# Optimization experiments

Measured on AMD Instinct MI355X. Metric: run time of the kernel, lower is better.

Reference implementation:

```python
import jax, jax.numpy as jnp
import numpy as np

N, C, D, G, FC0, FC1, TOPK = 1024, 2, 1024, 16, 64, 16, 10
DG = D // G  # 64, per-group dim for WQ/WK
OPG = D // G  # 64, conv output channels per group (dim[2]=1024, groups=16)


def setup_inputs() -> dict:
    key = jax.random.key(0)
    ks = jax.random.split(key, 11)
    s = 0.02
    return {
        "f_a": jax.random.normal(ks[0], (N, C, D), jnp.float32),
        "position_embedding": jax.random.uniform(ks[1], (C, N, N, FC0), jnp.float32),
        "iou": jax.random.uniform(ks[2], (C, N, N), jnp.float32),
        "WG_w": jax.random.normal(ks[3], (FC1, FC0), jnp.float32) * s,
        "WG_b": jnp.zeros((FC1,), jnp.float32),
        "WK_w": jax.random.normal(ks[4], (D, D), jnp.float32) * s,
        "WK_b": jnp.zeros((D,), jnp.float32),
        "WQ_w": jax.random.normal(ks[5], (D, D), jnp.float32) * s,
        "WQ_b": jnp.zeros((D,), jnp.float32),
        "conv_w": jax.random.normal(ks[6], (D, D), jnp.float32) * s,  # [out=1024, in_per_group=1024] (1x1 kernel squeezed)
        "conv_b": jnp.zeros((D,), jnp.float32),
    }


def reference(f_a, position_embedding, iou, WG_w, WG_b, WK_w, WK_b, WQ_w, WQ_b, conv_w, conv_b):
    n = f_a.shape[0]
    k = min(n, TOPK)
    fa = jnp.transpose(f_a, (1, 0, 2))  # [C, N, D]

    # geometric bias: relu(Linear) -> [C, N, N, G] -> [C, G, N, N]
    w_g = jax.nn.relu(jnp.einsum('cmne,oe->cmno', position_embedding, WG_w) + WG_b)
    w_g = jnp.transpose(w_g, (0, 3, 1, 2))  # [C, G, N, N]

    # multi-head Q/K with per-group dim DG
    w_k = (jnp.einsum('cnd,ed->cne', fa, WK_w) + WK_b).reshape(C, n, G, DG)
    w_q = (jnp.einsum('cnd,ed->cne', fa, WQ_w) + WQ_b).reshape(C, n, G, DG)
    aff = jnp.einsum('cngd,cmgd->cgnm', w_q, w_k) / jnp.sqrt(jnp.float32(DG))  # [C, G, N, N]

    # iou_method == 'b': iou >= 1e-6 -> log(1)=0, else log(1e-6)
    log_iou = jnp.where(iou >= 1e-6, jnp.float32(0.0), jnp.log(jnp.float32(1e-6)))[:, None, :, :]

    w_mn = jnp.log(jnp.clip(w_g, 1e-6, None)) + aff + log_iou  # [C, G, N, N]

    # topk -> softmax over topk -> scatter back into dense [C, G, N, N]
    vals, idx = jax.lax.top_k(w_mn, k)
    soft = jax.nn.softmax(vals, axis=-1)
    ci = jnp.arange(C)[:, None, None, None]
    gi = jnp.arange(G)[None, :, None, None]
    ri = jnp.arange(n)[None, None, :, None]
    attn = jnp.zeros_like(w_mn).at[ci, gi, ri, idx].set(soft)

    # sparse attention-weighted aggregation of values
    out = jnp.einsum('cgnm,cmd->cgnd', attn, fa)  # [C, G, N, D]

    # grouped 1x1 conv: group g maps its D input channels to OPG output channels
    Wr = conv_w.reshape(G, OPG, D)  # [g, o_local, i]
    y = jnp.einsum('goi,cgni->ncgo', Wr, out).reshape(n, C, G * OPG) + conv_b  # [N, C, 1024]
    return y
```

## Files before the change

kernel.cpp:

```cpp
#include <hip/hip_runtime.h>
#include <math.h>

#define NT 1024
#define CD 2
#define DD 1024
#define GG 16
#define LOG1E6 -13.8155105579642740f
#define NEG_BIG -1e30f

typedef short bf16x8 __attribute__((ext_vector_type(8)));
typedef float f32x4  __attribute__((ext_vector_type(4)));

__device__ __forceinline__ unsigned short bf16_rne(float x) {
    unsigned int u = __float_as_uint(x);
    unsigned int r = (u + 0x7fffu + ((u >> 16) & 1u)) >> 16;
    return (unsigned short)r;
}

__device__ __forceinline__ void split3_8(const float* v, bf16x8& h, bf16x8& m, bf16x8& l) {
    #pragma unroll
    for (int e = 0; e < 8; ++e) {
        const float x = v[e];
        const unsigned short hb = bf16_rne(x);
        const float hf = __uint_as_float((unsigned int)hb << 16);
        const float r1 = x - hf;
        const unsigned short mb = bf16_rne(r1);
        const float mf = __uint_as_float((unsigned int)mb << 16);
        const float r2 = r1 - mf;
        const unsigned short lb = bf16_rne(r2);
        h[e] = (short)hb; m[e] = (short)mb; l[e] = (short)lb;
    }
}

__global__ __launch_bounds__(256) void k1_proj(
    const float* __restrict__ fa,
    const float* __restrict__ Wq, const float* __restrict__ bq,
    const float* __restrict__ Wk, const float* __restrict__ bk,
    const float* __restrict__ Wc, const float* __restrict__ bc,
    float* __restrict__ Qo, float* __restrict__ Ko, float* __restrict__ Vo)
{
    const int et = blockIdx.x, rt = blockIdx.y, z = blockIdx.z;
    const float* W  = (z == 0) ? Wq : (z == 1) ? Wk : Wc;
    const float* bb = (z == 0) ? bq : (z == 1) ? bk : bc;
    float* Out      = (z == 0) ? Qo : (z == 1) ? Ko : Vo;

    __shared__ float Al[32][132];
    __shared__ float Wl[32][68];

    const int t  = threadIdx.x;
    const int tx = t & 15, ty = t >> 4;
    const int dd = t & 7,  rr = t >> 3;
    const int r0 = rt * 128, e0 = et * 64;

    float acc[8][4];
    #pragma unroll
    for (int a = 0; a < 8; ++a)
        #pragma unroll
        for (int b = 0; b < 4; ++b) acc[a][b] = 0.f;

    for (int kt = 0; kt < 32; ++kt) {
        const int db = kt * 32 + dd * 4;
        #pragma unroll
        for (int p = 0; p < 4; ++p) {
            const int row = rr + p * 32;
            const int r = r0 + row;
            const int n = r & (NT - 1), c = r >> 10;
            float4 a4 = *(const float4*)&fa[((size_t)(n * CD + c)) * DD + db];
            Al[dd*4+0][row] = a4.x; Al[dd*4+1][row] = a4.y;
            Al[dd*4+2][row] = a4.z; Al[dd*4+3][row] = a4.w;
        }
        #pragma unroll
        for (int p = 0; p < 2; ++p) {
            const int erow = rr + p * 32;
            float4 w4 = *(const float4*)&W[((size_t)(e0 + erow)) * DD + db];
            Wl[dd*4+0][erow] = w4.x; Wl[dd*4+1][erow] = w4.y;
            Wl[dd*4+2][erow] = w4.z; Wl[dd*4+3][erow] = w4.w;
        }
        __syncthreads();
        #pragma unroll 4
        for (int d = 0; d < 32; ++d) {
            float4 a0 = *(const float4*)&Al[d][ty * 8];
            float4 a1 = *(const float4*)&Al[d][ty * 8 + 4];
            float4 w4 = *(const float4*)&Wl[d][tx * 4];
            float av[8] = {a0.x, a0.y, a0.z, a0.w, a1.x, a1.y, a1.z, a1.w};
            float wv[4] = {w4.x, w4.y, w4.z, w4.w};
            #pragma unroll
            for (int a = 0; a < 8; ++a)
                #pragma unroll
                for (int b = 0; b < 4; ++b) acc[a][b] += av[a] * wv[b];
        }
        __syncthreads();
    }
    float4 b4 = *(const float4*)&bb[e0 + tx * 4];
    #pragma unroll
    for (int a = 0; a < 8; ++a) {
        float4 o;
        o.x = acc[a][0] + b4.x; o.y = acc[a][1] + b4.y;
        o.z = acc[a][2] + b4.z; o.w = acc[a][3] + b4.w;
        *(float4*)&Out[((size_t)(r0 + ty * 8 + a)) * DD + e0 + tx * 4] = o;
    }
}

__global__ __launch_bounds__(256) void k2a_aff(
    const float* __restrict__ Q, const float* __restrict__ Km,
    float* __restrict__ aff)
{
    const int jt = blockIdx.x, it = blockIdx.y, cg = blockIdx.z;
    const int c = cg >> 4, g = cg & 15;
    __shared__ float Ql[64][68];
    __shared__ float Kl[64][68];
    const int t = threadIdx.x;
    const int dd = t & 15, rr = t >> 4;
    const int i0 = it * 64, j0 = jt * 64;
    #pragma unroll
    for (int p = 0; p < 4; ++p) {
        const int row = rr + p * 16;
        float4 q4 = *(const float4*)&Q[((size_t)(c * NT + i0 + row)) * DD + g * 64 + dd * 4];
        Ql[dd*4+0][row] = q4.x; Ql[dd*4+1][row] = q4.y;
        Ql[dd*4+2][row] = q4.z; Ql[dd*4+3][row] = q4.w;
        float4 k4 = *(const float4*)&Km[((size_t)(c * NT + j0 + row)) * DD + g * 64 + dd * 4];
        Kl[dd*4+0][row] = k4.x; Kl[dd*4+1][row] = k4.y;
        Kl[dd*4+2][row] = k4.z; Kl[dd*4+3][row] = k4.w;
    }
    __syncthreads();
    const int tx = t & 15, ty = t >> 4;
    float acc[4][4];
    #pragma unroll
    for (int a = 0; a < 4; ++a)
        #pragma unroll
        for (int b = 0; b < 4; ++b) acc[a][b] = 0.f;
    #pragma unroll 8
    for (int d = 0; d < 64; ++d) {
        float4 q4 = *(const float4*)&Ql[d][ty * 4];
        float4 k4 = *(const float4*)&Kl[d][tx * 4];
        float qv[4] = {q4.x, q4.y, q4.z, q4.w};
        float kv[4] = {k4.x, k4.y, k4.z, k4.w};
        #pragma unroll
        for (int a = 0; a < 4; ++a)
            #pragma unroll
            for (int b = 0; b < 4; ++b) acc[a][b] += qv[a] * kv[b];
    }
    #pragma unroll
    for (int a = 0; a < 4; ++a) {
        float4 o;
        o.x = acc[a][0] * 0.125f; o.y = acc[a][1] * 0.125f;
        o.z = acc[a][2] * 0.125f; o.w = acc[a][3] * 0.125f;
        *(float4*)&aff[(((size_t)(c * GG + g)) * NT + i0 + ty * 4 + a) * NT + j0 + tx * 4] = o;
    }
}

__global__ __launch_bounds__(256, 4) void k3_scan(
    const float* __restrict__ pe, const float* __restrict__ iou,
    const float* __restrict__ WGw, const float* __restrict__ WGb,
    const float* __restrict__ aff,
    float* __restrict__ cv, int* __restrict__ ci)
{
    const int ch = blockIdx.x;
    const int it = blockIdx.y;
    const int c  = blockIdx.z;
    const int i0 = it * 8;

    __shared__ float wgl[8][16][33];
    __shared__ float ios[8][33];

    const int t = threadIdx.x;
    const int wave = t >> 6, lane = t & 63;
    const int lg = lane & 15, lk = lane >> 4;
    const int p_i = t >> 5, jq = t & 31;
    const int s_i = t >> 5, s_g = (t >> 1) & 15, s_h = t & 1;

    bf16x8 bh[2], bm[2], bl[2];
    #pragma unroll
    for (int kp = 0; kp < 2; ++kp) {
        float w8[8];
        float4 w0 = *(const float4*)&WGw[lg * 64 + kp * 32 + lk * 8];
        float4 w1 = *(const float4*)&WGw[lg * 64 + kp * 32 + lk * 8 + 4];
        w8[0]=w0.x; w8[1]=w0.y; w8[2]=w0.z; w8[3]=w0.w;
        w8[4]=w1.x; w8[5]=w1.y; w8[6]=w1.z; w8[7]=w1.w;
        split3_8(w8, bh[kp], bm[kp], bl[kp]);
    }
    const float bias = WGb[lg];

    float tv[10]; int tidx[10];
    #pragma unroll
    for (int q = 0; q < 10; ++q) { tv[q] = NEG_BIG; tidx[q] = 0; }

    for (int s = 0; s < 8; ++s) {
        const int j0 = ch * 256 + s * 32;
        {
            const float ia = iou[((size_t)c * NT + (i0 + p_i)) * NT + j0 + jq];
            ios[p_i][jq] = (ia >= 1e-6f) ? 0.f : LOG1E6;
        }
        #pragma unroll 1
        for (int rtt = 0; rtt < 4; ++rtt) {
            const int rt = wave * 4 + rtt;
            const int ib = rt >> 1;
            const int jb = (rt & 1) * 16;
            const float* pr = &pe[(((size_t)c * NT + (i0 + ib)) * NT + (j0 + jb + lg)) * 64];
            f32x4 acc = {0.f, 0.f, 0.f, 0.f};
            #pragma unroll
            for (int kp = 0; kp < 2; ++kp) {
                float a8[8];
                float4 v0 = *(const float4*)&pr[kp * 32 + lk * 8];
                float4 v1 = *(const float4*)&pr[kp * 32 + lk * 8 + 4];
                a8[0]=v0.x; a8[1]=v0.y; a8[2]=v0.z; a8[3]=v0.w;
                a8[4]=v1.x; a8[5]=v1.y; a8[6]=v1.z; a8[7]=v1.w;
                bf16x8 ah, am, al;
                split3_8(a8, ah, am, al);
                acc = __builtin_amdgcn_mfma_f32_16x16x32_bf16(al, bh[kp], acc, 0, 0, 0);
                acc = __builtin_amdgcn_mfma_f32_16x16x32_bf16(ah, bl[kp], acc, 0, 0, 0);
                acc = __builtin_amdgcn_mfma_f32_16x16x32_bf16(am, bm[kp], acc, 0, 0, 0);
                acc = __builtin_amdgcn_mfma_f32_16x16x32_bf16(am, bh[kp], acc, 0, 0, 0);
                acc = __builtin_amdgcn_mfma_f32_16x16x32_bf16(ah, bm[kp], acc, 0, 0, 0);
                acc = __builtin_amdgcn_mfma_f32_16x16x32_bf16(ah, bh[kp], acc, 0, 0, 0);
            }
            #pragma unroll
            for (int q = 0; q < 4; ++q) {
                const float v = acc[q] + bias;
                wgl[ib][lg][jb + lk * 4 + q] = (v > 1e-6f) ? __logf(v) : LOG1E6;
            }
        }
        __syncthreads();
        {
            const float* ar = &aff[(((size_t)(c * GG + s_g)) * NT + (i0 + s_i)) * NT + j0 + s_h * 16];
            const float* wl = &wgl[s_i][s_g][s_h * 16];
            const float* il = &ios[s_i][s_h * 16];
            #pragma unroll
            for (int j4 = 0; j4 < 16; j4 += 4) {
                float4 a4 = *(const float4*)&ar[j4];
                float av[4] = {a4.x, a4.y, a4.z, a4.w};
                #pragma unroll
                for (int q = 0; q < 4; ++q) {
                    const float val = wl[j4 + q] + av[q] + il[j4 + q];
                    if (val > tv[0]) {
                        const int ix = j0 + s_h * 16 + j4 + q;
                        #pragma unroll
                        for (int sl = 0; sl < 10; ++sl) {
                            const bool up   = (sl < 9) ? (val > tv[sl + 1]) : false;
                            const bool here = (val > tv[sl]);
                            const float ntv = up ? tv[sl + 1] : (here ? val : tv[sl]);
                            const int   nti = up ? tidx[sl + 1] : (here ? ix : tidx[sl]);
                            tv[sl] = ntv; tidx[sl] = nti;
                        }
                    }
                }
            }
        }
        __syncthreads();
    }

    float* mv = &wgl[0][0][0];
    int*   mi = (int*)(mv + 1280);
    const int pair = t >> 1;
    if (s_h == 1) {
        #pragma unroll
        for (int q = 0; q < 10; ++q) { mv[pair * 10 + q] = tv[q]; mi[pair * 10 + q] = tidx[q]; }
    }
    __syncthreads();
    if (s_h == 0) {
        for (int q = 9; q >= 0; --q) {
            const float val = mv[pair * 10 + q];
            const int   ix  = mi[pair * 10 + q];
            if (val > tv[0]) {
                #pragma unroll
                for (int sl = 0; sl < 10; ++sl) {
                    const bool up   = (sl < 9) ? (val > tv[sl + 1]) : false;
                    const bool here = (val > tv[sl]);
                    const float ntv = up ? tv[sl + 1] : (here ? val : tv[sl]);
                    const int   nti = up ? tidx[sl + 1] : (here ? ix : tidx[sl]);
                    tv[sl] = ntv; tidx[sl] = nti;
                }
            }
        }
        const size_t base = ((((size_t)c * NT + (i0 + s_i)) * GG + s_g) * 4 + ch) * 10;
        #pragma unroll
        for (int q = 0; q < 10; ++q) { cv[base + q] = tv[q]; ci[base + q] = tidx[q]; }
    }
}

__global__ __launch_bounds__(256) void k2b2_fin(
    const float* __restrict__ cv, const int* __restrict__ ci,
    const float* __restrict__ V, float* __restrict__ y)
{
    const int w    = (blockIdx.x << 2) + (threadIdx.x >> 6);
    const int lane = threadIdx.x & 63;
    const int c = w >> 14;
    const int i = (w >> 4) & (NT - 1);
    const int g = w & 15;

    float tv[10]; int tidx[10];
    #pragma unroll
    for (int q = 0; q < 10; ++q) { tv[q] = NEG_BIG; tidx[q] = 0; }

    const size_t base = (size_t)w * 40;
    for (int chn = 0; chn < 4; ++chn) {
        const float* cvp = &cv[base + chn * 10];
        const int*   cip = &ci[base + chn * 10];
        for (int q = 9; q >= 0; --q) {
            const float val = cvp[q];
            const int   ix  = cip[q];
            if (val > tv[0]) {
                #pragma unroll
                for (int sl = 0; sl < 10; ++sl) {
                    const bool up   = (sl < 9) ? (val > tv[sl + 1]) : false;
                    const bool here = (val > tv[sl]);
                    const float ntv = up ? tv[sl + 1] : (here ? val : tv[sl]);
                    const int   nti = up ? tidx[sl + 1] : (here ? ix : tidx[sl]);
                    tv[sl] = ntv; tidx[sl] = nti;
                }
            }
        }
    }
    const float m = tv[9];
    float wgt[10]; float sm = 0.f;
    #pragma unroll
    for (int q = 0; q < 10; ++q) { wgt[q] = __expf(tv[q] - m); sm += wgt[q]; }
    const float inv = 1.f / sm;
    float o = 0.f;
    #pragma unroll
    for (int q = 0; q < 10; ++q)
        o += (wgt[q] * inv) * V[((size_t)(c * NT + tidx[q])) * DD + g * 64 + lane];
    y[((size_t)i * CD + c) * DD + g * 64 + lane] = o;
}

extern "C" void kernel_launch(void* const* d_in, const int* in_sizes, int n_in,
                              void* d_out, int out_size, void* d_ws, size_t ws_size,
                              hipStream_t stream) {
    (void)in_sizes; (void)n_in; (void)out_size; (void)ws_size;
    const float* f_a = (const float*)d_in[0];
    const float* pe  = (const float*)d_in[1];
    const float* iou = (const float*)d_in[2];
    const float* WGw = (const float*)d_in[3];
    const float* WGb = (const float*)d_in[4];
    const float* WKw = (const float*)d_in[5];
    const float* WKb = (const float*)d_in[6];
    const float* WQw = (const float*)d_in[7];
    const float* WQb = (const float*)d_in[8];
    const float* Cw  = (const float*)d_in[9];
    const float* Cb  = (const float*)d_in[10];
    float* yout = (float*)d_out;

    float* ws  = (float*)d_ws;
    float* Q   = ws;
    float* Kp  = ws + (1u << 21);
    float* V   = ws + (2u << 21);
    float* aff = ws + (3u << 21);
    float* cv  = ws;
    int*   ci  = (int*)(ws + (1u << 21));

    k1_proj<<<dim3(16, 16, 3), 256, 0, stream>>>(f_a, WQw, WQb, WKw, WKb, Cw, Cb, Q, Kp, V);
    k2a_aff<<<dim3(16, 16, 32), 256, 0, stream>>>(Q, Kp, aff);
    k3_scan<<<dim3(4, 128, 2), 256, 0, stream>>>(pe, iou, WGw, WGb, aff, cv, ci);
    k2b2_fin<<<8192, 256, 0, stream>>>(cv, ci, V, yout);
}
```

Baseline: 512.5 us.

## Compute Q·K affinity with bf16x3 split MFMA instead of fp32 FMA tiles

The projection kernel now writes Q and K as three bf16 parts (high, mid, low) instead of fp32. The affinity kernel is replaced by one that keeps a 16-row Q tile in registers per wave and streams K tiles with a two-deep register prefetch, computing each 16x16 block with six bf16 MFMA products to approximate fp32 precision. This moves the per-group QK^T work from scalar FMAs onto matrix cores. In exchange Q/K storage and read traffic grows (three 16-bit planes instead of one 32-bit), and the output stores are scattered 4-byte writes along rows.

Result: slower. 535.8 us (+4.5%).

```diff
diff --git a/kernel.cpp b/kernel.cpp
--- a/kernel.cpp
+++ b/kernel.cpp
@@ -37,12 +37,16 @@
     const float* __restrict__ Wq, const float* __restrict__ bq,
     const float* __restrict__ Wk, const float* __restrict__ bk,
     const float* __restrict__ Wc, const float* __restrict__ bc,
-    float* __restrict__ Qo, float* __restrict__ Ko, float* __restrict__ Vo)
+    float* __restrict__ Vo,
+    unsigned short* __restrict__ Qh, unsigned short* __restrict__ Qm, unsigned short* __restrict__ Ql,
+    unsigned short* __restrict__ Kh, unsigned short* __restrict__ Km, unsigned short* __restrict__ Kl)
 {
     const int et = blockIdx.x, rt = blockIdx.y, z = blockIdx.z;
     const float* W  = (z == 0) ? Wq : (z == 1) ? Wk : Wc;
     const float* bb = (z == 0) ? bq : (z == 1) ? bk : bc;
-    float* Out      = (z == 0) ? Qo : (z == 1) ? Ko : Vo;
+    unsigned short* Sh = (z == 0) ? Qh : Kh;
+    unsigned short* Sm = (z == 0) ? Qm : Km;
+    unsigned short* Sl = (z == 0) ? Ql : Kl;
 
     __shared__ float Al[32][132];
     __shared__ float Wl[32][68];
@@ -94,58 +98,124 @@
     float4 b4 = *(const float4*)&bb[e0 + tx * 4];
     #pragma unroll
     for (int a = 0; a < 8; ++a) {
-        float4 o;
-        o.x = acc[a][0] + b4.x; o.y = acc[a][1] + b4.y;
-        o.z = acc[a][2] + b4.z; o.w = acc[a][3] + b4.w;
-        *(float4*)&Out[((size_t)(r0 + ty * 8 + a)) * DD + e0 + tx * 4] = o;
-    }
-}
-
-__global__ __launch_bounds__(256) void k2a_aff(
-    const float* __restrict__ Q, const float* __restrict__ Km,
+        float o[4];
+        o[0] = acc[a][0] + b4.x; o[1] = acc[a][1] + b4.y;
+        o[2] = acc[a][2] + b4.z; o[3] = acc[a][3] + b4.w;
+        const size_t idx = ((size_t)(r0 + ty * 8 + a)) * DD + e0 + tx * 4;
+        if (z == 2) {
+            *(float4*)&Vo[idx] = make_float4(o[0], o[1], o[2], o[3]);
+        } else {
+            ushort4 h4, m4, l4;
+            unsigned short hv[4], mv[4], lv[4];
+            #pragma unroll
+            for (int q = 0; q < 4; ++q) {
+                const float x = o[q];
+                const unsigned short hb = bf16_rne(x);
+                const float hf = __uint_as_float((unsigned int)hb << 16);
+                const float r1 = x - hf;
+                const unsigned short mb = bf16_rne(r1);
+                const float mf = __uint_as_float((unsigned int)mb << 16);
+                const unsigned short lb = bf16_rne(r1 - mf);
+                hv[q] = hb; mv[q] = mb; lv[q] = lb;
+            }
+            h4.x = hv[0]; h4.y = hv[1]; h4.z = hv[2]; h4.w = hv[3];
+            m4.x = mv[0]; m4.y = mv[1]; m4.z = mv[2]; m4.w = mv[3];
+            l4.x = lv[0]; l4.y = lv[1]; l4.z = lv[2]; l4.w = lv[3];
+            *(ushort4*)&Sh[idx] = h4;
+            *(ushort4*)&Sm[idx] = m4;
+            *(ushort4*)&Sl[idx] = l4;
+        }
+    }
+}
+
+__global__ __launch_bounds__(256) void k2a_mfma(
+    const unsigned short* __restrict__ Qh, const unsigned short* __restrict__ Qm,
+    const unsigned short* __restrict__ Ql,
+    const unsigned short* __restrict__ Kh, const unsigned short* __restrict__ Km,
+    const unsigned short* __restrict__ Kl,
     float* __restrict__ aff)
 {
-    const int jt = blockIdx.x, it = blockIdx.y, cg = blockIdx.z;
+    const int jh = blockIdx.x;
+    const int itg = blockIdx.y;
+    const int cg = blockIdx.z;
     const int c = cg >> 4, g = cg & 15;
-    __shared__ float Ql[64][68];
-    __shared__ float Kl[64][68];
-    const int t = threadIdx.x;
-    const int dd = t & 15, rr = t >> 4;
-    const int i0 = it * 64, j0 = jt * 64;
-    #pragma unroll
-    for (int p = 0; p < 4; ++p) {
-        const int row = rr + p * 16;
-        float4 q4 = *(const float4*)&Q[((size_t)(c * NT + i0 + row)) * DD + g * 64 + dd * 4];
-        Ql[dd*4+0][row] = q4.x; Ql[dd*4+1][row] = q4.y;
-        Ql[dd*4+2][row] = q4.z; Ql[dd*4+3][row] = q4.w;
-        float4 k4 = *(const float4*)&Km[((size_t)(c * NT + j0 + row)) * DD + g * 64 + dd * 4];
-        Kl[dd*4+0][row] = k4.x; Kl[dd*4+1][row] = k4.y;
-        Kl[dd*4+2][row] = k4.z; Kl[dd*4+3][row] = k4.w;
-    }
-    __syncthreads();
-    const int tx = t & 15, ty = t >> 4;
-    float acc[4][4];
-    #pragma unroll
-    for (int a = 0; a < 4; ++a)
-        #pragma unroll
-        for (int b = 0; b < 4; ++b) acc[a][b] = 0.f;
-    #pragma unroll 8
-    for (int d = 0; d < 64; ++d) {
-        float4 q4 = *(const float4*)&Ql[d][ty * 4];
-        float4 k4 = *(const float4*)&Kl[d][tx * 4];
-        float qv[4] = {q4.x, q4.y, q4.z, q4.w};
-        float kv[4] = {k4.x, k4.y, k4.z, k4.w};
-        #pragma unroll
-        for (int a = 0; a < 4; ++a)
-            #pragma unroll
-            for (int b = 0; b < 4; ++b) acc[a][b] += qv[a] * kv[b];
-    }
-    #pragma unroll
-    for (int a = 0; a < 4; ++a) {
-        float4 o;
-        o.x = acc[a][0] * 0.125f; o.y = acc[a][1] * 0.125f;
-        o.z = acc[a][2] * 0.125f; o.w = acc[a][3] * 0.125f;
-        *(float4*)&aff[(((size_t)(c * GG + g)) * NT + i0 + ty * 4 + a) * NT + j0 + tx * 4] = o;
+    const int w = threadIdx.x >> 6, lane = threadIdx.x & 63;
+    const int lg = lane & 15, lk = lane >> 4;
+    const int i0 = (itg * 4 + w) * 16;
+
+    const size_t qb = ((size_t)(c * NT + i0 + lg)) * DD + g * 64 + lk * 8;
+    bf16x8 qh[2], qm[2], ql[2];
+    #pragma unroll
+    for (int kp = 0; kp < 2; ++kp) {
+        qh[kp] = *(const bf16x8*)&Qh[qb + kp * 32];
+        qm[kp] = *(const bf16x8*)&Qm[qb + kp * 32];
+        ql[kp] = *(const bf16x8*)&Ql[qb + kp * 32];
+    }
+
+    const size_t kb0 = ((size_t)(c * NT + jh * 512 + lg)) * DD + g * 64 + lk * 8;
+    const size_t jstride = (size_t)16 * DD;
+
+    bf16x8 kAh[2], kAm[2], kAl[2], kBh[2], kBm[2], kBl[2];
+    #pragma unroll
+    for (int kp = 0; kp < 2; ++kp) {
+        kAh[kp] = *(const bf16x8*)&Kh[kb0 + kp * 32];
+        kAm[kp] = *(const bf16x8*)&Km[kb0 + kp * 32];
+        kAl[kp] = *(const bf16x8*)&Kl[kb0 + kp * 32];
+    }
+
+    const int j0base = jh * 512;
+    #pragma unroll 1
+    for (int jt = 0; jt < 32; jt += 2) {
+        {
+            const size_t kb = kb0 + (size_t)(jt + 1) * jstride;
+            #pragma unroll
+            for (int kp = 0; kp < 2; ++kp) {
+                kBh[kp] = *(const bf16x8*)&Kh[kb + kp * 32];
+                kBm[kp] = *(const bf16x8*)&Km[kb + kp * 32];
+                kBl[kp] = *(const bf16x8*)&Kl[kb + kp * 32];
+            }
+        }
+        {
+            f32x4 acc = {0.f, 0.f, 0.f, 0.f};
+            #pragma unroll
+            for (int kp = 0; kp < 2; ++kp) {
+                acc = __builtin_amdgcn_mfma_f32_16x16x32_bf16(ql[kp], kAh[kp], acc, 0, 0, 0);
+                acc = __builtin_amdgcn_mfma_f32_16x16x32_bf16(qh[kp], kAl[kp], acc, 0, 0, 0);
+                acc = __builtin_amdgcn_mfma_f32_16x16x32_bf16(qm[kp], kAm[kp], acc, 0, 0, 0);
+                acc = __builtin_amdgcn_mfma_f32_16x16x32_bf16(qm[kp], kAh[kp], acc, 0, 0, 0);
+                acc = __builtin_amdgcn_mfma_f32_16x16x32_bf16(qh[kp], kAm[kp], acc, 0, 0, 0);
+                acc = __builtin_amdgcn_mfma_f32_16x16x32_bf16(qh[kp], kAh[kp], acc, 0, 0, 0);
+            }
+            const int j0 = j0base + jt * 16;
+            #pragma unroll
+            for (int q = 0; q < 4; ++q)
+                aff[((size_t)cg * NT + i0 + lk * 4 + q) * NT + j0 + lg] = acc[q] * 0.125f;
+        }
+        if (jt + 2 < 32) {
+            const size_t kb = kb0 + (size_t)(jt + 2) * jstride;
+            #pragma unroll
+            for (int kp = 0; kp < 2; ++kp) {
+                kAh[kp] = *(const bf16x8*)&Kh[kb + kp * 32];
+                kAm[kp] = *(const bf16x8*)&Km[kb + kp * 32];
+                kAl[kp] = *(const bf16x8*)&Kl[kb + kp * 32];
+            }
+        }
+        {
+            f32x4 acc = {0.f, 0.f, 0.f, 0.f};
+            #pragma unroll
+            for (int kp = 0; kp < 2; ++kp) {
+                acc = __builtin_amdgcn_mfma_f32_16x16x32_bf16(ql[kp], kBh[kp], acc, 0, 0, 0);
+                acc = __builtin_amdgcn_mfma_f32_16x16x32_bf16(qh[kp], kBl[kp], acc, 0, 0, 0);
+                acc = __builtin_amdgcn_mfma_f32_16x16x32_bf16(qm[kp], kBm[kp], acc, 0, 0, 0);
+                acc = __builtin_amdgcn_mfma_f32_16x16x32_bf16(qm[kp], kBh[kp], acc, 0, 0, 0);
+                acc = __builtin_amdgcn_mfma_f32_16x16x32_bf16(qh[kp], kBm[kp], acc, 0, 0, 0);
+                acc = __builtin_amdgcn_mfma_f32_16x16x32_bf16(qh[kp], kBh[kp], acc, 0, 0, 0);
+            }
+            const int j0 = j0base + (jt + 1) * 16;
+            #pragma unroll
+            for (int q = 0; q < 4; ++q)
+                aff[((size_t)cg * NT + i0 + lk * 4 + q) * NT + j0 + lg] = acc[q] * 0.125f;
+        }
     }
 }
 
@@ -341,15 +411,22 @@
     float* yout = (float*)d_out;
 
     float* ws  = (float*)d_ws;
-    float* Q   = ws;
-    float* Kp  = ws + (1u << 21);
     float* V   = ws + (2u << 21);
     float* aff = ws + (3u << 21);
     float* cv  = ws;
     int*   ci  = (int*)(ws + (1u << 21));
-
-    k1_proj<<<dim3(16, 16, 3), 256, 0, stream>>>(f_a, WQw, WQb, WKw, WKb, Cw, Cb, Q, Kp, V);
-    k2a_aff<<<dim3(16, 16, 32), 256, 0, stream>>>(Q, Kp, aff);
+    unsigned short* sp = (unsigned short*)(ws + (3u << 21) + (1u << 25));
+    const size_t SPN = (size_t)CD * NT * DD;
+    unsigned short* Qh = sp;
+    unsigned short* Qm = sp + SPN;
+    unsigned short* Ql = sp + 2 * SPN;
+    unsigned short* Kh = sp + 3 * SPN;
+    unsigned short* Km = sp + 4 * SPN;
+    unsigned short* Kl = sp + 5 * SPN;
+
+    k1_proj<<<dim3(16, 16, 3), 256, 0, stream>>>(f_a, WQw, WQb, WKw, WKb, Cw, Cb,
+                                                 V, Qh, Qm, Ql, Kh, Km, Kl);
+    k2a_mfma<<<dim3(2, 16, 32), 256, 0, stream>>>(Qh, Qm, Ql, Kh, Km, Kl, aff);
     k3_scan<<<dim3(4, 128, 2), 256, 0, stream>>>(pe, iou, WGw, WGb, aff, cv, ci);
     k2b2_fin<<<8192, 256, 0, stream>>>(cv, ci, V, yout);
 }
```

## Move projection GEMMs to bf16x3 split MFMA with a pre-split kernel

Applied to the files above, without the earlier changes.

Adds a kernel that splits f_a and the three weight matrices into high, mid and low bf16 parts. The Q/K/V projection then runs as six-term bf16 MFMA products to emulate fp32 accuracy, replacing the scalar FMA GEMM. The aim is to cut the cost of the roughly 12 GFLOP projection by using matrix cores. The price is an extra kernel launch, about 36MB of extra split-data traffic, and uncoalesced scalar output stores.

New measurement: 426.3 us. 16.8% less time.

```diff
diff --git a/kernel.cpp b/kernel.cpp
--- a/kernel.cpp
+++ b/kernel.cpp
@@ -32,72 +32,144 @@
     }
 }
 
-__global__ __launch_bounds__(256) void k1_proj(
-    const float* __restrict__ fa,
-    const float* __restrict__ Wq, const float* __restrict__ bq,
-    const float* __restrict__ Wk, const float* __restrict__ bk,
-    const float* __restrict__ Wc, const float* __restrict__ bc,
+__global__ __launch_bounds__(256) void k0_split(
+    const float* __restrict__ fa, const float* __restrict__ Wq,
+    const float* __restrict__ Wk, const float* __restrict__ Wc,
+    unsigned short* __restrict__ Fh, unsigned short* __restrict__ Fm, unsigned short* __restrict__ Fl,
+    unsigned short* __restrict__ WQh, unsigned short* __restrict__ WQm, unsigned short* __restrict__ WQl,
+    unsigned short* __restrict__ WKh, unsigned short* __restrict__ WKm, unsigned short* __restrict__ WKl,
+    unsigned short* __restrict__ WCh, unsigned short* __restrict__ WCm, unsigned short* __restrict__ WCl)
+{
+    const int reg = blockIdx.y;
+    const float* src = (reg == 0) ? fa : (reg == 1) ? Wq : (reg == 2) ? Wk : Wc;
+    unsigned short* dh = (reg == 0) ? Fh : (reg == 1) ? WQh : (reg == 2) ? WKh : WCh;
+    unsigned short* dm = (reg == 0) ? Fm : (reg == 1) ? WQm : (reg == 2) ? WKm : WCm;
+    unsigned short* dl = (reg == 0) ? Fl : (reg == 1) ? WQl : (reg == 2) ? WKl : WCl;
+    const int nv = (reg == 0) ? (1 << 19) : (1 << 18);
+
+    for (int v = blockIdx.x * 256 + threadIdx.x; v < nv; v += gridDim.x * 256) {
+        float4 x4 = *(const float4*)&src[(size_t)v * 4];
+        float xv[4] = {x4.x, x4.y, x4.z, x4.w};
+        ushort4 h4, m4, l4;
+        unsigned short hv[4], mv[4], lv[4];
+        #pragma unroll
+        for (int q = 0; q < 4; ++q) {
+            const float x = xv[q];
+            const unsigned short hb = bf16_rne(x);
+            const float hf = __uint_as_float((unsigned int)hb << 16);
+            const float r1 = x - hf;
+            const unsigned short mb = bf16_rne(r1);
+            const float mf = __uint_as_float((unsigned int)mb << 16);
+            const unsigned short lb = bf16_rne(r1 - mf);
+            hv[q] = hb; mv[q] = mb; lv[q] = lb;
+        }
+        h4.x = hv[0]; h4.y = hv[1]; h4.z = hv[2]; h4.w = hv[3];
+        m4.x = mv[0]; m4.y = mv[1]; m4.z = mv[2]; m4.w = mv[3];
+        l4.x = lv[0]; l4.y = lv[1]; l4.z = lv[2]; l4.w = lv[3];
+        *(ushort4*)&dh[(size_t)v * 4] = h4;
+        *(ushort4*)&dm[(size_t)v * 4] = m4;
+        *(ushort4*)&dl[(size_t)v * 4] = l4;
+    }
+}
+
+__global__ __launch_bounds__(256) void k1_mfma(
+    const unsigned short* __restrict__ Fh, const unsigned short* __restrict__ Fm,
+    const unsigned short* __restrict__ Fl,
+    const unsigned short* __restrict__ WQh, const unsigned short* __restrict__ WQm,
+    const unsigned short* __restrict__ WQl,
+    const unsigned short* __restrict__ WKh, const unsigned short* __restrict__ WKm,
+    const unsigned short* __restrict__ WKl,
+    const unsigned short* __restrict__ WCh, const unsigned short* __restrict__ WCm,
+    const unsigned short* __restrict__ WCl,
+    const float* __restrict__ bq, const float* __restrict__ bk, const float* __restrict__ bc,
     float* __restrict__ Qo, float* __restrict__ Ko, float* __restrict__ Vo)
 {
     const int et = blockIdx.x, rt = blockIdx.y, z = blockIdx.z;
-    const float* W  = (z == 0) ? Wq : (z == 1) ? Wk : Wc;
+    const unsigned short* Wh = (z == 0) ? WQh : (z == 1) ? WKh : WCh;
+    const unsigned short* Wm = (z == 0) ? WQm : (z == 1) ? WKm : WCm;
+    const unsigned short* Wl = (z == 0) ? WQl : (z == 1) ? WKl : WCl;
     const float* bb = (z == 0) ? bq : (z == 1) ? bk : bc;
     float* Out      = (z == 0) ? Qo : (z == 1) ? Ko : Vo;
 
-    __shared__ float Al[32][132];
-    __shared__ float Wl[32][68];
-
-    const int t  = threadIdx.x;
-    const int tx = t & 15, ty = t >> 4;
-    const int dd = t & 7,  rr = t >> 3;
-    const int r0 = rt * 128, e0 = et * 64;
-
-    float acc[8][4];
-    #pragma unroll
-    for (int a = 0; a < 8; ++a)
-        #pragma unroll
-        for (int b = 0; b < 4; ++b) acc[a][b] = 0.f;
+    const int c  = rt >> 3;
+    const int n0 = (rt & 7) * 128;
+    const int r0 = rt * 128;
+    const int e0 = et * 64;
+
+    __shared__ unsigned short Ah[128][36], Am[128][36], Al[128][36];
+    __shared__ unsigned short Bh[64][36],  Bm[64][36],  Bl[64][36];
+
+    const int t    = threadIdx.x;
+    const int wave = t >> 6, lane = t & 63;
+    const int wr   = wave >> 1, wc = wave & 1;
+    const int lrow = lane & 15, lk = lane >> 4;
+
+    f32x4 acc[4][2];
+    #pragma unroll
+    for (int m = 0; m < 4; ++m)
+        #pragma unroll
+        for (int n = 0; n < 2; ++n) acc[m][n] = (f32x4){0.f, 0.f, 0.f, 0.f};
 
     for (int kt = 0; kt < 32; ++kt) {
-        const int db = kt * 32 + dd * 4;
-        #pragma unroll
-        for (int p = 0; p < 4; ++p) {
-            const int row = rr + p * 32;
-            const int r = r0 + row;
-            const int n = r & (NT - 1), c = r >> 10;
-            float4 a4 = *(const float4*)&fa[((size_t)(n * CD + c)) * DD + db];
-            Al[dd*4+0][row] = a4.x; Al[dd*4+1][row] = a4.y;
-            Al[dd*4+2][row] = a4.z; Al[dd*4+3][row] = a4.w;
-        }
+        const int kb = kt * 32;
         #pragma unroll
         for (int p = 0; p < 2; ++p) {
-            const int erow = rr + p * 32;
-            float4 w4 = *(const float4*)&W[((size_t)(e0 + erow)) * DD + db];
-            Wl[dd*4+0][erow] = w4.x; Wl[dd*4+1][erow] = w4.y;
-            Wl[dd*4+2][erow] = w4.z; Wl[dd*4+3][erow] = w4.w;
+            const int task = t + p * 256;
+            const int row = task >> 2, seg = task & 3;
+            const size_t gs = ((size_t)((n0 + row) * CD + c)) * DD + kb + seg * 8;
+            *(uint4*)&Ah[row][seg * 8] = *(const uint4*)&Fh[gs];
+            *(uint4*)&Am[row][seg * 8] = *(const uint4*)&Fm[gs];
+            *(uint4*)&Al[row][seg * 8] = *(const uint4*)&Fl[gs];
+        }
+        {
+            const int row = t >> 2, seg = t & 3;
+            const size_t gs = ((size_t)(e0 + row)) * DD + kb + seg * 8;
+            *(uint4*)&Bh[row][seg * 8] = *(const uint4*)&Wh[gs];
+            *(uint4*)&Bm[row][seg * 8] = *(const uint4*)&Wm[gs];
+            *(uint4*)&Bl[row][seg * 8] = *(const uint4*)&Wl[gs];
         }
         __syncthreads();
-        #pragma unroll 4
-        for (int d = 0; d < 32; ++d) {
-            float4 a0 = *(const float4*)&Al[d][ty * 8];
-            float4 a1 = *(const float4*)&Al[d][ty * 8 + 4];
-            float4 w4 = *(const float4*)&Wl[d][tx * 4];
-            float av[8] = {a0.x, a0.y, a0.z, a0.w, a1.x, a1.y, a1.z, a1.w};
-            float wv[4] = {w4.x, w4.y, w4.z, w4.w};
-            #pragma unroll
-            for (int a = 0; a < 8; ++a)
+        {
+            bf16x8 ah[4], am[4], al[4], bh[2], bm[2], bl[2];
+            #pragma unroll
+            for (int m = 0; m < 4; ++m) {
+                const int row = wr * 64 + m * 16 + lrow;
+                ah[m] = *(const bf16x8*)&Ah[row][lk * 8];
+                am[m] = *(const bf16x8*)&Am[row][lk * 8];
+                al[m] = *(const bf16x8*)&Al[row][lk * 8];
+            }
+            #pragma unroll
+            for (int n = 0; n < 2; ++n) {
+                const int row = wc * 32 + n * 16 + lrow;
+                bh[n] = *(const bf16x8*)&Bh[row][lk * 8];
+                bm[n] = *(const bf16x8*)&Bm[row][lk * 8];
+                bl[n] = *(const bf16x8*)&Bl[row][lk * 8];
+            }
+            #pragma unroll
+            for (int m = 0; m < 4; ++m)
                 #pragma unroll
-                for (int b = 0; b < 4; ++b) acc[a][b] += av[a] * wv[b];
+                for (int n = 0; n < 2; ++n) {
+                    acc[m][n] = __builtin_amdgcn_mfma_f32_16x16x32_bf16(al[m], bh[n], acc[m][n], 0, 0, 0);
+                    acc[m][n] = __builtin_amdgcn_mfma_f32_16x16x32_bf16(ah[m], bl[n], acc[m][n], 0, 0, 0);
+                    acc[m][n] = __builtin_amdgcn_mfma_f32_16x16x32_bf16(am[m], bm[n], acc[m][n], 0, 0, 0);
+                    acc[m][n] = __builtin_amdgcn_mfma_f32_16x16x32_bf16(am[m], bh[n], acc[m][n], 0, 0, 0);
+                    acc[m][n] = __builtin_amdgcn_mfma_f32_16x16x32_bf16(ah[m], bm[n], acc[m][n], 0, 0, 0);
+                    acc[m][n] = __builtin_amdgcn_mfma_f32_16x16x32_bf16(ah[m], bh[n], acc[m][n], 0, 0, 0);
+                }
         }
         __syncthreads();
     }
-    float4 b4 = *(const float4*)&bb[e0 + tx * 4];
-    #pragma unroll
-    for (int a = 0; a < 8; ++a) {
-        float4 o;
-        o.x = acc[a][0] + b4.x; o.y = acc[a][1] + b4.y;
-        o.z = acc[a][2] + b4.z; o.w = acc[a][3] + b4.w;
-        *(float4*)&Out[((size_t)(r0 + ty * 8 + a)) * DD + e0 + tx * 4] = o;
+    #pragma unroll
+    for (int n = 0; n < 2; ++n) {
+        const int e = e0 + wc * 32 + n * 16 + lrow;
+        const float bias = bb[e];
+        #pragma unroll
+        for (int m = 0; m < 4; ++m) {
+            const int r = r0 + wr * 64 + m * 16 + lk * 4;
+            #pragma unroll
+            for (int q = 0; q < 4; ++q)
+                Out[((size_t)(r + q)) * DD + e] = acc[m][n][q] + bias;
+        }
     }
 }
 
@@ -347,8 +419,27 @@
     float* aff = ws + (3u << 21);
     float* cv  = ws;
     int*   ci  = (int*)(ws + (1u << 21));
-
-    k1_proj<<<dim3(16, 16, 3), 256, 0, stream>>>(f_a, WQw, WQb, WKw, WKb, Cw, Cb, Q, Kp, V);
+    unsigned short* sp = (unsigned short*)(ws + (3u << 21) + (1u << 25));
+    const size_t FN = (size_t)CD * NT * DD;
+    const size_t WN = (size_t)DD * DD / 1;
+    unsigned short* Fh  = sp;
+    unsigned short* Fm  = Fh + FN;
+    unsigned short* Fl  = Fm + FN;
+    unsigned short* WQh = Fl + FN;
+    unsigned short* WQm = WQh + WN;
+    unsigned short* WQl = WQm + WN;
+    unsigned short* WKh = WQl + WN;
+    unsigned short* WKm = WKh + WN;
+    unsigned short* WKl = WKm + WN;
+    unsigned short* WCh = WKl + WN;
+    unsigned short* WCm = WCh + WN;
+    unsigned short* WCl = WCm + WN;
+
+    k0_split<<<dim3(512, 4), 256, 0, stream>>>(f_a, WQw, WKw, Cw,
+        Fh, Fm, Fl, WQh, WQm, WQl, WKh, WKm, WKl, WCh, WCm, WCl);
+    k1_mfma<<<dim3(16, 16, 3), 256, 0, stream>>>(
+        Fh, Fm, Fl, WQh, WQm, WQl, WKh, WKm, WKl, WCh, WCm, WCl,
+        WQb, WKb, Cb, Q, Kp, V);
     k2a_aff<<<dim3(16, 16, 32), 256, 0, stream>>>(Q, Kp, aff);
     k3_scan<<<dim3(4, 128, 2), 256, 0, stream>>>(pe, iou, WGw, WGb, aff, cv, ci);
     k2b2_fin<<<8192, 256, 0, stream>>>(cv, ci, V, yout);
```
